# Performance work log

Hardware: AMD Instinct MI355X
Metric: run time of the kernel (lower is better)

Reference implementation:

```python
import jax, jax.numpy as jnp
import numpy as np

B, T, DMODEL = 2, 2048, 1024
H, DK, DV = 16, 64, 64
FF = 4096
EPS = 1e-5


def _layernorm_2d(x):
    # torch LayerNorm(normalized_shape=(T, dmodel)): normalize jointly over last two
    # dims, biased variance, weight=1 / bias=0 (freshly constructed each forward).
    mu = jnp.mean(x, axis=(1, 2), keepdims=True)
    var = jnp.mean((x - mu) ** 2, axis=(1, 2), keepdims=True)
    return (x - mu) / jnp.sqrt(var + EPS)


def setup_inputs() -> dict:
    key = jax.random.key(0)
    ks = jax.random.split(key, 9)
    s = 0.02  # small init for numerical sanity (original uses uniform(-1,1))
    return {
        "x": jax.random.normal(ks[0], (B, T, DMODEL), jnp.float32),
        "Wq": jax.random.normal(ks[1], (H, DMODEL, DK), jnp.float32) * s,
        "Wk": jax.random.normal(ks[2], (H, DMODEL, DK), jnp.float32) * s,
        "Wv": jax.random.normal(ks[3], (H, DMODEL, DV), jnp.float32) * s,
        "Wo": jax.random.normal(ks[4], (DMODEL, DMODEL), jnp.float32) * s,
        "W1": jax.random.normal(ks[5], (DMODEL, FF), jnp.float32) * s,
        "b1": jnp.zeros((FF,), jnp.float32),
        "W2": jax.random.normal(ks[6], (FF, DMODEL), jnp.float32) * s,
        "b2": jnp.zeros((DMODEL,), jnp.float32),
    }


def reference(x, Wq, Wk, Wv, Wo, W1, b1, W2, b2):
    b, t, d = x.shape
    h, _, dk = Wq.shape
    dv = Wv.shape[-1]
    # per-head projections: (B,H,T,dk/dv)
    Qp = jnp.einsum("btd,hdk->bhtk", x, Wq)
    Kp = jnp.einsum("btd,hdk->bhtk", x, Wk)
    Vp = jnp.einsum("btd,hdv->bhtv", x, Wv)
    scores = jnp.einsum("bhqk,bhsk->bhqs", Qp, Kp) / np.sqrt(dk).astype(np.float32)
    # NOTE: original does torch.softmax(heads, 2) -> softmax over the QUERY axis
    attn = jax.nn.softmax(scores, axis=2)
    heads = jnp.einsum("bhqs,bhsv->bqhv", attn, Vp).reshape(b, t, h * dv)
    att_out = heads @ Wo
    o1 = _layernorm_2d(x + att_out)
    ff = jnp.maximum(o1 @ W1 + b1, 0.0) @ W2 + b2
    return _layernorm_2d(o1 + ff)
```

## Files before the change

kernel.cpp:

```cpp
#include <hip/hip_runtime.h>
#include <hip/hip_bf16.h>
#include <cstddef>
#include <cstdint>

typedef __hip_bfloat16 hbf;
typedef __attribute__((ext_vector_type(8))) __bf16 bf16x8;
typedef __attribute__((ext_vector_type(4))) float f32x4;

#define B_ 2
#define T_ 2048
#define D_ 1024
#define H_ 16
#define FF_ 4096
#define EPS_ 1e-5f
#define SCALE_ 0.18033688011112f

__device__ __forceinline__ float bf2f(hbf v) { return __bfloat162float(v); }
__device__ __forceinline__ float fexp2(float x) {
  return __builtin_amdgcn_exp2f(x);
}
__device__ __forceinline__ float flog2(float x) {
  return __builtin_amdgcn_logf(x);
}
__device__ __forceinline__ float ldin(const void* p, size_t i, int isbf) {
  return isbf ? __bfloat162float(((const hbf*)p)[i]) : ((const float*)p)[i];
}
__device__ __forceinline__ void ston(void* p, size_t i, float v, int isbf) {
  if (isbf) ((hbf*)p)[i] = __float2bfloat16(v);
  else ((float*)p)[i] = v;
}
__device__ __forceinline__ f32x4 mfma16(bf16x8 a, bf16x8 b, f32x4 c) {
  return __builtin_amdgcn_mfma_f32_16x16x32_bf16(a, b, c, 0, 0, 0);
}
__device__ __forceinline__ bf16x8 ldfrag(const hbf* p) {
  return *(const bf16x8*)p;
}
__device__ __forceinline__ void glds16(const hbf* g, hbf* l) {
  __builtin_amdgcn_global_load_lds(
      (const __attribute__((address_space(1))) void*)g,
      (__attribute__((address_space(3))) void*)l, 16, 0, 0);
}

__global__ __launch_bounds__(256) void detect_dtype(const unsigned* x,
                                                    int* flag) {
  __shared__ int cnt[256];
  int c = 0;
  for (int i = threadIdx.x; i < 4096; i += 256) {
    unsigned low = x[i] & 0xFFFFu;
    unsigned e = (low >> 7) & 0xFFu;
    if (e >= 100u && e <= 142u) c++;
  }
  cnt[threadIdx.x] = c;
  __syncthreads();
  for (int off = 128; off > 0; off >>= 1) {
    if ((int)threadIdx.x < off) cnt[threadIdx.x] += cnt[threadIdx.x + off];
    __syncthreads();
  }
  if (threadIdx.x == 0) *flag = (cnt[0] > 2458) ? 1 : 0;
}

__device__ __forceinline__ void tr_tile(const void* __restrict__ src,
                                        hbf* __restrict__ dst, int R, int C,
                                        size_t zoff, int cx, int ry, int f,
                                        float (*tile)[33]) {
  const int tx = threadIdx.x & 31, ty = threadIdx.x >> 5;
  const int c0 = cx * 32, r0 = ry * 32;
#pragma unroll
  for (int p = 0; p < 4; p++) {
    int rr = p * 8 + ty;
    tile[rr][tx] = ldin(src, zoff + (size_t)(r0 + rr) * C + c0 + tx, f);
  }
  __syncthreads();
#pragma unroll
  for (int p = 0; p < 4; p++) {
    int cc = p * 8 + ty;
    dst[zoff + (size_t)(c0 + cc) * R + r0 + tx] = __float2bfloat16(tile[tx][cc]);
  }
}

__global__ __launch_bounds__(256) void preconv(
    const void* __restrict__ x, const void* __restrict__ Wq,
    const void* __restrict__ Wk, const void* __restrict__ Wv,
    const void* __restrict__ Wo, const void* __restrict__ W1,
    const void* __restrict__ W2, const void* __restrict__ b1,
    const void* __restrict__ b2, hbf* __restrict__ xb,
    hbf* __restrict__ wqkvt, hbf* __restrict__ wot, hbf* __restrict__ w1t,
    hbf* __restrict__ w2t, hbf* __restrict__ b1b, hbf* __restrict__ b2b,
    const int* __restrict__ flag) {
  __shared__ float tile[32][33];
  const int f = *flag;
  const int bid = blockIdx.x;
  if (bid < 3072) {
    int which = bid >> 10;
    int r = bid & 1023;
    int z = r >> 6, rem = r & 63;
    int ry = rem >> 1, cx = rem & 1;
    const void* src = (which == 0) ? Wq : (which == 1) ? Wk : Wv;
    hbf* dst = wqkvt + (size_t)which * (D_ * D_);
    tr_tile(src, dst, 1024, 64, (size_t)z * 65536, cx, ry, f, tile);
  } else if (bid < 4096) {
    int t = bid - 3072;
    tr_tile(Wo, wot, 1024, 1024, 0, t & 31, t >> 5, f, tile);
  } else if (bid < 8192) {
    int t = bid - 4096;
    tr_tile(W1, w1t, 1024, 4096, 0, t & 127, t >> 7, f, tile);
  } else if (bid < 12288) {
    int t = bid - 8192;
    tr_tile(W2, w2t, 4096, 1024, 0, t & 31, t >> 5, f, tile);
  } else if (bid < 13312) {
    size_t base = (size_t)(bid - 12288) * 4096;
    if (f) {
      const uint4* src = (const uint4*)((const hbf*)x + base);
      uint4* dst = (uint4*)(xb + base);
      for (int i = threadIdx.x; i < 512; i += 256) dst[i] = src[i];
    } else {
      const float4* src = (const float4*)((const float*)x + base);
      for (int i = threadIdx.x; i < 512; i += 256) {
        float4 a = src[i * 2], b = src[i * 2 + 1];
        union {
          hbf h[8];
          uint4 u;
        } o;
        o.h[0] = __float2bfloat16(a.x);
        o.h[1] = __float2bfloat16(a.y);
        o.h[2] = __float2bfloat16(a.z);
        o.h[3] = __float2bfloat16(a.w);
        o.h[4] = __float2bfloat16(b.x);
        o.h[5] = __float2bfloat16(b.y);
        o.h[6] = __float2bfloat16(b.z);
        o.h[7] = __float2bfloat16(b.w);
        *(uint4*)(xb + base + (size_t)i * 8) = o.u;
      }
    }
  } else if (bid == 13312) {
    for (int i = threadIdx.x; i < FF_; i += 256)
      b1b[i] = __float2bfloat16(ldin(b1, i, f));
  } else {
    for (int i = threadIdx.x; i < D_; i += 256)
      b2b[i] = __float2bfloat16(ldin(b2, i, f));
  }
}

template <int MODE, int BM, int BN>
__global__ __launch_bounds__(256) void gemm_bt(
    const hbf* __restrict__ A, const hbf* __restrict__ Bt, hbf* __restrict__ C,
    float* __restrict__ Cf0, float* __restrict__ Cf1,
    const hbf* __restrict__ e1, float* __restrict__ red, int M, int N, int K,
    int LDK) {
  constexpr int WM = BM / 2, WN = BN / 2;
  constexpr int IF = WM / 16, JF = WN / 16;
  __shared__ alignas(16) hbf As[BM * 64];
  __shared__ alignas(16) hbf Bs[BN * 64];
  const int tid = threadIdx.x;
  const int wave = tid >> 6, lane = tid & 63;
  const int quad = lane >> 4, l16 = lane & 15;
  const int m0 = blockIdx.y * BM, n0 = blockIdx.x * BN;
  const int mw = (wave >> 1) * WM, nw = (wave & 1) * WN;
  const int srow = tid >> 3;
  const int scol = (tid & 7) * 8;
  const int kbase = (MODE == 4) ? blockIdx.z * K : 0;
  const f32x4 zero = {0.f, 0.f, 0.f, 0.f};
  f32x4 acc[IF][JF];
#pragma unroll
  for (int i = 0; i < IF; i++)
#pragma unroll
    for (int j = 0; j < JF; j++) acc[i][j] = zero;

  const hbf* ga = &A[(size_t)(m0 + srow) * LDK + kbase + scol];
  const hbf* gb = &Bt[(size_t)(n0 + srow) * LDK + kbase + scol];
  hbf* lA = &As[wave * 512];
  hbf* lB = &Bs[wave * 512];

  for (int k0 = 0; k0 < K; k0 += 64) {
#pragma unroll
    for (int c = 0; c < BM / 32; c++)
      glds16(ga + (size_t)(c * 32) * LDK + k0, lA + c * 2048);
#pragma unroll
    for (int c = 0; c < BN / 32; c++)
      glds16(gb + (size_t)(c * 32) * LDK + k0, lB + c * 2048);
    __syncthreads();
    bf16x8 af[2][IF], bfr[2][JF];
#pragma unroll
    for (int h = 0; h < 2; h++) {
#pragma unroll
      for (int i = 0; i < IF; i++)
        af[h][i] = ldfrag(&As[(mw + i * 16 + l16) * 64 + h * 32 + quad * 8]);
#pragma unroll
      for (int j = 0; j < JF; j++)
        bfr[h][j] = ldfrag(&Bs[(nw + j * 16 + l16) * 64 + h * 32 + quad * 8]);
    }
#pragma unroll
    for (int h = 0; h < 2; h++)
#pragma unroll
      for (int i = 0; i < IF; i++)
#pragma unroll
        for (int j = 0; j < JF; j++)
          acc[i][j] = mfma16(af[h][i], bfr[h][j], acc[i][j]);
    __syncthreads();
  }
  float ssum = 0.f, ssq = 0.f;
#pragma unroll
  for (int i = 0; i < IF; i++)
#pragma unroll
    for (int j = 0; j < JF; j++)
#pragma unroll
      for (int r = 0; r < 4; r++) {
        int m = m0 + mw + i * 16 + quad * 4 + r;
        int n = n0 + nw + j * 16 + l16;
        float v = acc[i][j][r];
        if (MODE == 0) {
          int which = n >> 10, n1 = n & 1023;
          int h = n1 >> 6, cc = n1 & 63;
          int b = m >> 11, t = m & (T_ - 1);
          if (which == 0) v *= SCALE_;
          C[(size_t)which * ((size_t)B_ * H_ * T_ * 64) +
            (((size_t)(b * H_ + h)) * T_ + t) * 64 + cc] = __float2bfloat16(v);
        } else if (MODE == 1) {
          hbf hv = __float2bfloat16(v + bf2f(e1[(size_t)m * N + n]));
          C[(size_t)m * N + n] = hv;
          float fv = bf2f(hv);
          ssum += fv;
          ssq += fv * fv;
        } else if (MODE == 2) {
          C[(size_t)m * N + n] = __float2bfloat16(fmaxf(v + bf2f(e1[n]), 0.f));
        } else if (MODE == 4) {
          float* Cf = blockIdx.z ? Cf1 : Cf0;
          Cf[(size_t)m * N + n] = v;
        }
      }
  if (MODE == 1) {
    float* sc = (float*)As;
    sc[tid] = ssum;
    sc[256 + tid] = ssq;
    __syncthreads();
    for (int off = 128; off > 0; off >>= 1) {
      if (tid < off) {
        sc[tid] += sc[tid + off];
        sc[256 + tid] += sc[256 + tid + off];
      }
      __syncthreads();
    }
    if (tid == 0) {
      int b = m0 >> 11;
      atomicAdd(&red[b * 2 + 0], sc[0]);
      atomicAdd(&red[b * 2 + 1], sc[256]);
    }
  }
}

__global__ __launch_bounds__(256) void attn_stats(const hbf* __restrict__ Q,
                                                  const hbf* __restrict__ K,
                                                  const hbf* __restrict__ V,
                                                  hbf* __restrict__ Vt) {
  __shared__ alignas(16) hbf Ks[64 * 72];
  __shared__ alignas(16) hbf Qs[64 * 72];
  __shared__ float sAdj[64];
  const int bh = blockIdx.y;
  const int s0 = blockIdx.x * 64;
  const int tid = threadIdx.x;
  const int wave = tid >> 6, lane = tid & 63;
  const int quad = lane >> 4, l16 = lane & 15;
  const int sw = wave * 16;
  const hbf* Kb = K + (size_t)bh * T_ * 64;
  const hbf* Qb = Q + (size_t)bh * T_ * 64;
  const hbf* Vb = V + (size_t)bh * T_ * 64;
  hbf* Vtb = Vt + (size_t)bh * 64 * T_;
  const int r_ = tid >> 3, c_ = (tid & 7) * 8;
#pragma unroll
  for (int c = 0; c < 2; c++) {
    int row = c * 32 + r_;
    *(float4*)(&Ks[row * 72 + c_]) =
        *(const float4*)(&Kb[(size_t)(s0 + row) * 64 + c_]);
  }
  __syncthreads();
  bf16x8 kf0 = ldfrag(&Ks[(sw + l16) * 72 + quad * 8]);
  bf16x8 kf1 = ldfrag(&Ks[(sw + l16) * 72 + 32 + quad * 8]);
  float m_thr[4], l_thr[4];
#pragma unroll
  for (int r = 0; r < 4; r++) {
    m_thr[r] = -1e30f;
    l_thr[r] = 0.f;
  }
  const f32x4 zero = {0.f, 0.f, 0.f, 0.f};
  for (int qt = 0; qt < T_ / 64; qt++) {
    if (qt) __syncthreads();
#pragma unroll
    for (int c = 0; c < 2; c++) {
      int row = c * 32 + r_;
      *(float4*)(&Qs[row * 72 + c_]) =
          *(const float4*)(&Qb[(size_t)(qt * 64 + row) * 64 + c_]);
    }
    __syncthreads();
    f32x4 acc[4];
#pragma unroll
    for (int j = 0; j < 4; j++) {
      bf16x8 qf0 = ldfrag(&Qs[(j * 16 + l16) * 72 + quad * 8]);
      bf16x8 qf1 = ldfrag(&Qs[(j * 16 + l16) * 72 + 32 + quad * 8]);
      f32x4 a = zero;
      a = mfma16(kf0, qf0, a);
      a = mfma16(kf1, qf1, a);
      acc[j] = a;
    }
#pragma unroll
    for (int r = 0; r < 4; r++) {
      float mt = fmaxf(fmaxf(acc[0][r], acc[1][r]),
                       fmaxf(acc[2][r], acc[3][r]));
      float nm = fmaxf(m_thr[r], mt);
      float s = l_thr[r] * fexp2(m_thr[r] - nm);
#pragma unroll
      for (int j = 0; j < 4; j++) s += fexp2(acc[j][r] - nm);
      l_thr[r] = s;
      m_thr[r] = nm;
    }
  }
#pragma unroll
  for (int d = 1; d < 16; d <<= 1) {
#pragma unroll
    for (int r = 0; r < 4; r++) {
      float om = __shfl_xor(m_thr[r], d);
      float ol = __shfl_xor(l_thr[r], d);
      float nm = fmaxf(m_thr[r], om);
      l_thr[r] = l_thr[r] * fexp2(m_thr[r] - nm) + ol * fexp2(om - nm);
      m_thr[r] = nm;
    }
  }
  if (l16 == 0) {
#pragma unroll
    for (int r = 0; r < 4; r++)
      sAdj[sw + quad * 4 + r] = m_thr[r] + flog2(l_thr[r]);
  }
  __syncthreads();
#pragma unroll
  for (int c = 0; c < 2; c++) {
    int e = (c * 256 + tid) * 8;
    int r = e >> 6, col = e & 63;
    union alignas(16) {
      hbf h[8];
      float4 f4;
    } u;
    u.f4 = *(const float4*)(&Vb[(size_t)(s0 + r) * 64 + col]);
    float sc = fexp2(-sAdj[r]);
#pragma unroll
    for (int k2 = 0; k2 < 8; k2++)
      u.h[k2] = __float2bfloat16(bf2f(u.h[k2]) * sc);
    *(float4*)(&Ks[r * 72 + col]) = u.f4;
  }
  __syncthreads();
#pragma unroll
  for (int c = 0; c < 2; c++) {
    int e = (c * 256 + tid) * 8;
    int v = e >> 6, tt = e & 63;
    union alignas(16) {
      hbf h[8];
      float4 f4;
    } u;
#pragma unroll
    for (int k2 = 0; k2 < 8; k2++) u.h[k2] = Ks[(tt + k2) * 72 + v];
    *(float4*)(&Vtb[(size_t)v * T_ + s0 + tt]) = u.f4;
  }
}

__global__ __launch_bounds__(256) void attn_apply(const hbf* __restrict__ Q,
                                                  const hbf* __restrict__ K,
                                                  const hbf* __restrict__ Vt,
                                                  hbf* __restrict__ heads) {
  __shared__ alignas(16) hbf Ksb[2 * 64 * 64];
  __shared__ alignas(16) hbf Vsb[3 * 64 * 64];
  __shared__ alignas(16) hbf Ps[4 * 2 * 32 * 72];
  const int bh = blockIdx.y;
  const int b = bh >> 4, h = bh & 15;
  const int q0 = blockIdx.x * 128;
  const int tid = threadIdx.x;
  const int wave = tid >> 6, lane = tid & 63;
  const int quad = lane >> 4, l16 = lane & 15;
  const int qw = wave * 32;
  const hbf* Qb = Q + (size_t)bh * T_ * 64;
  const hbf* Kb = K + (size_t)bh * T_ * 64;
  const hbf* Vtb = Vt + (size_t)bh * 64 * T_;
  hbf* Pw = &Ps[wave * (2 * 32 * 72)];
  const int srow = tid >> 3, sc8 = tid & 7;
  const int swz = sc8 ^ (srow & 7);
  const hbf* gk = Kb + (size_t)srow * 64 + swz * 8;
  const hbf* gv = Vtb + (size_t)srow * T_ + swz * 8;
  hbf* lK = &Ksb[wave * 512];
  hbf* lV = &Vsb[wave * 512];
  const int sx = (l16 & 7) * 8;
  bf16x8 qf[2][2];
#pragma unroll
  for (int i = 0; i < 2; i++)
#pragma unroll
    for (int hh = 0; hh < 2; hh++)
      qf[i][hh] = ldfrag(&Qb[(size_t)(q0 + qw + i * 16 + l16) * 64 + hh * 32 +
                             quad * 8]);
  const f32x4 zero = {0.f, 0.f, 0.f, 0.f};
  f32x4 accO[2][4];
#pragma unroll
  for (int i = 0; i < 2; i++)
#pragma unroll
    for (int j = 0; j < 4; j++) accO[i][j] = zero;

  glds16(gk, lK);
  glds16(gk + 2048, lK + 2048);
  glds16(gv, lV);
  glds16(gv + (size_t)32 * T_, lV + 2048);
  glds16(gk + 4096, lK + 4096);
  glds16(gk + 4096 + 2048, lK + 4096 + 2048);
  glds16(gv + 64, lV + 4096);
  glds16(gv + (size_t)32 * T_ + 64, lV + 4096 + 2048);
  __syncthreads();

  {
    const hbf* Kc = &Ksb[0];
    bf16x8 kf[4][2];
#pragma unroll
    for (int j = 0; j < 4; j++)
#pragma unroll
      for (int hh = 0; hh < 2; hh++)
        kf[j][hh] =
            ldfrag(&Kc[(j * 16 + l16) * 64 + ((hh * 32 + quad * 8) ^ sx)]);
    __builtin_amdgcn_s_setprio(1);
    f32x4 accS[2][4];
#pragma unroll
    for (int i = 0; i < 2; i++)
#pragma unroll
      for (int j = 0; j < 4; j++) {
        f32x4 a = mfma16(kf[j][0], qf[i][0], zero);
        accS[i][j] = mfma16(kf[j][1], qf[i][1], a);
      }
    __builtin_amdgcn_s_setprio(0);
#pragma unroll
    for (int i = 0; i < 2; i++)
#pragma unroll
      for (int j = 0; j < 4; j++) {
        union {
          hbf h4[4];
          uint2 u;
        } pk;
#pragma unroll
        for (int r = 0; r < 4; r++)
          pk.h4[r] = __float2bfloat16(fexp2(accS[i][j][r]));
        *(uint2*)&Pw[(i * 16 + l16) * 72 + j * 16 + quad * 4] = pk.u;
      }
  }
  __syncthreads();

  for (int st = 1; st < T_ / 64; st++) {
    const int kcur = st & 1;
    const int pcur = st & 1, pprev = pcur ^ 1;
    const int vprev = (st - 1) % 3;
    if (st < T_ / 64 - 1) {
      const int knxt = (st + 1) & 1, vnxt = (st + 1) % 3;
      size_t ko = (size_t)(st + 1) * 4096;
      glds16(gk + ko, lK + knxt * 4096);
      glds16(gk + ko + 2048, lK + knxt * 4096 + 2048);
      glds16(gv + (st + 1) * 64, lV + vnxt * 4096);
      glds16(gv + (size_t)32 * T_ + (st + 1) * 64, lV + vnxt * 4096 + 2048);
    }
    const hbf* Kc = &Ksb[kcur * 4096];
    const hbf* Vp = &Vsb[vprev * 4096];
    bf16x8 kf[4][2];
#pragma unroll
    for (int j = 0; j < 4; j++)
#pragma unroll
      for (int hh = 0; hh < 2; hh++)
        kf[j][hh] =
            ldfrag(&Kc[(j * 16 + l16) * 64 + ((hh * 32 + quad * 8) ^ sx)]);
    bf16x8 pf[2][2];
#pragma unroll
    for (int i = 0; i < 2; i++)
#pragma unroll
      for (int hh = 0; hh < 2; hh++)
        pf[i][hh] = ldfrag(
            &Pw[pprev * (32 * 72) + (i * 16 + l16) * 72 + hh * 32 + quad * 8]);
    __builtin_amdgcn_s_setprio(1);
#pragma unroll
    for (int j2 = 0; j2 < 4; j2++) {
      bf16x8 vf0 = ldfrag(&Vp[(j2 * 16 + l16) * 64 + ((quad * 8) ^ sx)]);
      bf16x8 vf1 = ldfrag(&Vp[(j2 * 16 + l16) * 64 + ((32 + quad * 8) ^ sx)]);
#pragma unroll
      for (int i = 0; i < 2; i++) {
        accO[i][j2] = mfma16(pf[i][0], vf0, accO[i][j2]);
        accO[i][j2] = mfma16(pf[i][1], vf1, accO[i][j2]);
      }
    }
    f32x4 accS[2][4];
#pragma unroll
    for (int i = 0; i < 2; i++)
#pragma unroll
      for (int j = 0; j < 4; j++) {
        f32x4 a = mfma16(kf[j][0], qf[i][0], zero);
        accS[i][j] = mfma16(kf[j][1], qf[i][1], a);
      }
    __builtin_amdgcn_s_setprio(0);
#pragma unroll
    for (int i = 0; i < 2; i++)
#pragma unroll
      for (int j = 0; j < 4; j++) {
        union {
          hbf h4[4];
          uint2 u;
        } pk;
#pragma unroll
        for (int r = 0; r < 4; r++)
          pk.h4[r] = __float2bfloat16(fexp2(accS[i][j][r]));
        *(uint2*)&Pw[pcur * (32 * 72) + (i * 16 + l16) * 72 + j * 16 +
                     quad * 4] = pk.u;
      }
    __syncthreads();
  }
  {
    const int pl = (T_ / 64 - 1) & 1;
    const hbf* Vp = &Vsb[((T_ / 64 - 1) % 3) * 4096];
    bf16x8 pf[2][2];
#pragma unroll
    for (int i = 0; i < 2; i++)
#pragma unroll
      for (int hh = 0; hh < 2; hh++)
        pf[i][hh] = ldfrag(
            &Pw[pl * (32 * 72) + (i * 16 + l16) * 72 + hh * 32 + quad * 8]);
    __builtin_amdgcn_s_setprio(1);
#pragma unroll
    for (int j2 = 0; j2 < 4; j2++) {
      bf16x8 vf0 = ldfrag(&Vp[(j2 * 16 + l16) * 64 + ((quad * 8) ^ sx)]);
      bf16x8 vf1 = ldfrag(&Vp[(j2 * 16 + l16) * 64 + ((32 + quad * 8) ^ sx)]);
#pragma unroll
      for (int i = 0; i < 2; i++) {
        accO[i][j2] = mfma16(pf[i][0], vf0, accO[i][j2]);
        accO[i][j2] = mfma16(pf[i][1], vf1, accO[i][j2]);
      }
    }
    __builtin_amdgcn_s_setprio(0);
  }
#pragma unroll
  for (int i = 0; i < 2; i++)
#pragma unroll
    for (int j2 = 0; j2 < 4; j2++)
#pragma unroll
      for (int r = 0; r < 4; r++) {
        int q = q0 + qw + i * 16 + quad * 4 + r;
        int v = j2 * 16 + l16;
        heads[((size_t)(b * T_ + q)) * D_ + h * 64 + v] =
            __float2bfloat16(accO[i][j2][r]);
      }
}

__global__ __launch_bounds__(256) void ln_norm(const hbf* __restrict__ src,
                                               const float* __restrict__ red,
                                               void* dst,
                                               const int* __restrict__ flag,
                                               int force_bf) {
  const int isbf = force_bf ? 1 : *flag;
  const float invN = 1.f / (float)(T_ * D_);
  for (size_t i = (size_t)blockIdx.x * 256 + threadIdx.x;
       i < (size_t)B_ * T_ * D_; i += (size_t)gridDim.x * 256) {
    int b = (int)(i >> 21);
    float mu = red[b * 2 + 0] * invN;
    float var = red[b * 2 + 1] * invN - mu * mu;
    ston(dst, i, (bf2f(src[i]) - mu) * rsqrtf(var + EPS_), isbf);
  }
}

__global__ __launch_bounds__(256) void ln2_stats(const float* __restrict__ P0,
                                                 const float* __restrict__ P1,
                                                 const hbf* __restrict__ o1,
                                                 const hbf* __restrict__ b2b,
                                                 float* __restrict__ red) {
  __shared__ float s1[256], s2[256];
  const int b = blockIdx.y;
  const size_t base = (size_t)b * (T_ * D_);
  float sum = 0.f, sq = 0.f;
  for (size_t i = (size_t)blockIdx.x * 256 + threadIdx.x; i < (size_t)T_ * D_;
       i += (size_t)gridDim.x * 256) {
    size_t e = base + i;
    float v = P0[e] + P1[e] + bf2f(b2b[i & (D_ - 1)]) + bf2f(o1[e]);
    sum += v;
    sq += v * v;
  }
  s1[threadIdx.x] = sum;
  s2[threadIdx.x] = sq;
  __syncthreads();
  for (int off = 128; off > 0; off >>= 1) {
    if ((int)threadIdx.x < off) {
      s1[threadIdx.x] += s1[threadIdx.x + off];
      s2[threadIdx.x] += s2[threadIdx.x + off];
    }
    __syncthreads();
  }
  if (threadIdx.x == 0) {
    atomicAdd(&red[b * 2 + 0], s1[0]);
    atomicAdd(&red[b * 2 + 1], s2[0]);
  }
}

__global__ __launch_bounds__(256) void ln2_norm(
    const float* __restrict__ P0, const float* __restrict__ P1,
    const hbf* __restrict__ o1, const hbf* __restrict__ b2b,
    const float* __restrict__ red, void* dst, const int* __restrict__ flag) {
  const int isbf = *flag;
  const float invN = 1.f / (float)(T_ * D_);
  for (size_t i = (size_t)blockIdx.x * 256 + threadIdx.x;
       i < (size_t)B_ * T_ * D_; i += (size_t)gridDim.x * 256) {
    int b = (int)(i >> 21);
    float mu = red[b * 2 + 0] * invN;
    float var = red[b * 2 + 1] * invN - mu * mu;
    float v = P0[i] + P1[i] + bf2f(b2b[i & (D_ - 1)]) + bf2f(o1[i]);
    ston(dst, i, (v - mu) * rsqrtf(var + EPS_), isbf);
  }
}

extern "C" void kernel_launch(void* const* d_in, const int* in_sizes, int n_in,
                              void* d_out, int out_size, void* d_ws,
                              size_t ws_size, hipStream_t stream) {
  const void* x = d_in[0];
  const void* Wq = d_in[1];
  const void* Wk = d_in[2];
  const void* Wv = d_in[3];
  const void* Wo = d_in[4];
  const void* W1 = d_in[5];
  const void* W2 = d_in[7];
  const void* b1 = d_in[6];
  const void* b2 = d_in[8];

  const size_t MB = 1024 * 1024;
  if (ws_size < 89 * MB) return;

  char* w = (char*)d_ws;
  hbf* xb = (hbf*)(w + 0 * MB);
  hbf* wqkvt = (hbf*)(w + 8 * MB);
  hbf* wot = (hbf*)(w + 14 * MB);
  hbf* w1t = (hbf*)(w + 16 * MB);
  hbf* w2t = (hbf*)(w + 24 * MB);
  hbf* Qb = (hbf*)(w + 32 * MB);
  hbf* Kb = (hbf*)(w + 40 * MB);
  hbf* Vb = (hbf*)(w + 48 * MB);
  hbf* Vtb = (hbf*)(w + 56 * MB);
  hbf* heads = (hbf*)(w + 64 * MB);
  hbf* r1 = (hbf*)(w + 72 * MB);
  hbf* o1 = (hbf*)(w + 80 * MB);
  hbf* ff1 = (hbf*)(w + 32 * MB);
  float* P0 = (float*)(w + 0 * MB);
  float* P1 = (float*)(w + 64 * MB);
  hbf* b1b = (hbf*)(w + 88 * MB);
  hbf* b2b = b1b + FF_;
  float* red = (float*)(b2b + D_);
  int* flag = (int*)(red + 8);

  hipMemsetAsync(red, 0, 8 * sizeof(float) + sizeof(int), stream);
  detect_dtype<<<1, 256, 0, stream>>>((const unsigned*)x, flag);

  const int M = B_ * T_;
  preconv<<<13314, 256, 0, stream>>>(x, Wq, Wk, Wv, Wo, W1, W2, b1, b2, xb,
                                     wqkvt, wot, w1t, w2t, b1b, b2b, flag);
  gemm_bt<0, 128, 128><<<dim3(24, 32), 256, 0, stream>>>(
      xb, wqkvt, Qb, nullptr, nullptr, nullptr, nullptr, M, 3 * D_, D_, D_);
  attn_stats<<<dim3(32, 32), 256, 0, stream>>>(Qb, Kb, Vb, Vtb);
  attn_apply<<<dim3(16, 32), 256, 0, stream>>>(Qb, Kb, Vtb, heads);
  gemm_bt<1, 128, 64><<<dim3(16, 32), 256, 0, stream>>>(
      heads, wot, r1, nullptr, nullptr, xb, red, M, D_, D_, D_);
  ln_norm<<<4096, 256, 0, stream>>>(r1, red, o1, flag, 1);
  gemm_bt<2, 128, 128><<<dim3(32, 32), 256, 0, stream>>>(
      o1, w1t, ff1, nullptr, nullptr, b1b, nullptr, M, FF_, D_, D_);
  gemm_bt<4, 128, 128><<<dim3(8, 32, 2), 256, 0, stream>>>(
      ff1, w2t, nullptr, P0, P1, nullptr, nullptr, M, D_, FF_ / 2, FF_);
  ln2_stats<<<dim3(256, B_), 256, 0, stream>>>(P0, P1, o1, b2b, red + 4);
  ln2_norm<<<2048, 256, 0, stream>>>(P0, P1, o1, b2b, red + 4, d_out, flag);
}
```

Before: 452.5 us.

## Swizzle GEMM block order, transpose MFMA output for vector stores, vectorize LN2

Adds an XCD-aware block-index swizzle to three of the GEMMs so that neighbouring tiles land on the same chiplet, aiming for better L2 reuse. Swaps the MFMA operand order so each lane holds four consecutive columns, which lets every epilogue write packed 8-byte or 16-byte vectors instead of scalar stores. Also vectorizes the final layernorm stats and normalize kernels with float4 and packed bf16 loads and stores. The swizzle assumes the block count divides evenly by 8, and the new output mapping must match the transposed fragment layout.

```diff
diff --git a/kernel.cpp b/kernel.cpp
--- a/kernel.cpp
+++ b/kernel.cpp
@@ -141,7 +141,7 @@
   }
 }
 
-template <int MODE, int BM, int BN>
+template <int MODE, int BM, int BN, int SWZ>
 __global__ __launch_bounds__(256) void gemm_bt(
     const hbf* __restrict__ A, const hbf* __restrict__ Bt, hbf* __restrict__ C,
     float* __restrict__ Cf0, float* __restrict__ Cf1,
@@ -154,7 +154,17 @@
   const int tid = threadIdx.x;
   const int wave = tid >> 6, lane = tid & 63;
   const int quad = lane >> 4, l16 = lane & 15;
-  const int m0 = blockIdx.y * BM, n0 = blockIdx.x * BN;
+  int bx = blockIdx.x, by = blockIdx.y;
+  if (SWZ) {
+    const int gx = gridDim.x;
+    const int nwg = gx * gridDim.y;
+    const int flat = by * gx + bx;
+    const int cpx = nwg >> 3;
+    const int f2 = (flat & 7) * cpx + (flat >> 3);
+    bx = f2 % gx;
+    by = f2 / gx;
+  }
+  const int m0 = by * BM, n0 = bx * BN;
   const int mw = (wave >> 1) * WM, nw = (wave & 1) * WN;
   const int srow = tid >> 3;
   const int scol = (tid & 7) * 8;
@@ -195,39 +205,60 @@
       for (int i = 0; i < IF; i++)
 #pragma unroll
         for (int j = 0; j < JF; j++)
-          acc[i][j] = mfma16(af[h][i], bfr[h][j], acc[i][j]);
+          acc[i][j] = mfma16(bfr[h][j], af[h][i], acc[i][j]);
     __syncthreads();
   }
   float ssum = 0.f, ssq = 0.f;
 #pragma unroll
   for (int i = 0; i < IF; i++)
 #pragma unroll
-    for (int j = 0; j < JF; j++)
-#pragma unroll
-      for (int r = 0; r < 4; r++) {
-        int m = m0 + mw + i * 16 + quad * 4 + r;
-        int n = n0 + nw + j * 16 + l16;
-        float v = acc[i][j][r];
-        if (MODE == 0) {
-          int which = n >> 10, n1 = n & 1023;
-          int h = n1 >> 6, cc = n1 & 63;
-          int b = m >> 11, t = m & (T_ - 1);
-          if (which == 0) v *= SCALE_;
-          C[(size_t)which * ((size_t)B_ * H_ * T_ * 64) +
-            (((size_t)(b * H_ + h)) * T_ + t) * 64 + cc] = __float2bfloat16(v);
-        } else if (MODE == 1) {
-          hbf hv = __float2bfloat16(v + bf2f(e1[(size_t)m * N + n]));
-          C[(size_t)m * N + n] = hv;
+    for (int j = 0; j < JF; j++) {
+      const int m = m0 + mw + i * 16 + l16;
+      const int n = n0 + nw + j * 16 + quad * 4;
+      const f32x4 v = acc[i][j];
+      if (MODE == 0) {
+        int which = n >> 10, n1 = n & 1023;
+        int h = n1 >> 6, cc = n1 & 63;
+        int b = m >> 11, t = m & (T_ - 1);
+        float sc = (which == 0) ? SCALE_ : 1.f;
+        union {
+          hbf h4[4];
+          uint2 u;
+        } pk;
+#pragma unroll
+        for (int r = 0; r < 4; r++) pk.h4[r] = __float2bfloat16(v[r] * sc);
+        *(uint2*)&C[(size_t)which * ((size_t)B_ * H_ * T_ * 64) +
+                    (((size_t)(b * H_ + h)) * T_ + t) * 64 + cc] = pk.u;
+      } else if (MODE == 1) {
+        union {
+          hbf h4[4];
+          uint2 u;
+        } e, o;
+        e.u = *(const uint2*)&e1[(size_t)m * N + n];
+#pragma unroll
+        for (int r = 0; r < 4; r++) {
+          hbf hv = __float2bfloat16(v[r] + bf2f(e.h4[r]));
+          o.h4[r] = hv;
           float fv = bf2f(hv);
           ssum += fv;
           ssq += fv * fv;
-        } else if (MODE == 2) {
-          C[(size_t)m * N + n] = __float2bfloat16(fmaxf(v + bf2f(e1[n]), 0.f));
-        } else if (MODE == 4) {
-          float* Cf = blockIdx.z ? Cf1 : Cf0;
-          Cf[(size_t)m * N + n] = v;
         }
-      }
+        *(uint2*)&C[(size_t)m * N + n] = o.u;
+      } else if (MODE == 2) {
+        union {
+          hbf h4[4];
+          uint2 u;
+        } e, o;
+        e.u = *(const uint2*)&e1[n];
+#pragma unroll
+        for (int r = 0; r < 4; r++)
+          o.h4[r] = __float2bfloat16(fmaxf(v[r] + bf2f(e.h4[r]), 0.f));
+        *(uint2*)&C[(size_t)m * N + n] = o.u;
+      } else if (MODE == 4) {
+        float* Cf = blockIdx.z ? Cf1 : Cf0;
+        *(f32x4*)&Cf[(size_t)m * N + n] = v;
+      }
+    }
   if (MODE == 1) {
     float* sc = (float*)As;
     sc[tid] = ssum;
@@ -567,14 +598,27 @@
                                                  float* __restrict__ red) {
   __shared__ float s1[256], s2[256];
   const int b = blockIdx.y;
-  const size_t base = (size_t)b * (T_ * D_);
+  const size_t base = (size_t)b * (T_ * D_ / 4);
+  const float4* P0v = (const float4*)P0;
+  const float4* P1v = (const float4*)P1;
+  const uint2* o1v = (const uint2*)o1;
+  const uint2* b2v = (const uint2*)b2b;
   float sum = 0.f, sq = 0.f;
-  for (size_t i = (size_t)blockIdx.x * 256 + threadIdx.x; i < (size_t)T_ * D_;
-       i += (size_t)gridDim.x * 256) {
-    size_t e = base + i;
-    float v = P0[e] + P1[e] + bf2f(b2b[i & (D_ - 1)]) + bf2f(o1[e]);
-    sum += v;
-    sq += v * v;
+  for (size_t i = (size_t)blockIdx.x * 256 + threadIdx.x;
+       i < (size_t)(T_ * D_ / 4); i += (size_t)gridDim.x * 256) {
+    float4 p0 = P0v[base + i], p1 = P1v[base + i];
+    union {
+      uint2 u;
+      hbf h[4];
+    } o, bb;
+    o.u = o1v[base + i];
+    bb.u = b2v[i & (D_ / 4 - 1)];
+#pragma unroll
+    for (int r = 0; r < 4; r++) {
+      float v = (&p0.x)[r] + (&p1.x)[r] + bf2f(bb.h[r]) + bf2f(o.h[r]);
+      sum += v;
+      sq += v * v;
+    }
   }
   s1[threadIdx.x] = sum;
   s2[threadIdx.x] = sq;
@@ -598,13 +642,40 @@
     const float* __restrict__ red, void* dst, const int* __restrict__ flag) {
   const int isbf = *flag;
   const float invN = 1.f / (float)(T_ * D_);
+  const float4* P0v = (const float4*)P0;
+  const float4* P1v = (const float4*)P1;
+  const uint2* o1v = (const uint2*)o1;
+  const uint2* b2v = (const uint2*)b2b;
   for (size_t i = (size_t)blockIdx.x * 256 + threadIdx.x;
-       i < (size_t)B_ * T_ * D_; i += (size_t)gridDim.x * 256) {
-    int b = (int)(i >> 21);
+       i < (size_t)B_ * T_ * D_ / 4; i += (size_t)gridDim.x * 256) {
+    int b = (int)(i >> 19);
     float mu = red[b * 2 + 0] * invN;
     float var = red[b * 2 + 1] * invN - mu * mu;
-    float v = P0[i] + P1[i] + bf2f(b2b[i & (D_ - 1)]) + bf2f(o1[i]);
-    ston(dst, i, (v - mu) * rsqrtf(var + EPS_), isbf);
+    float rstd = rsqrtf(var + EPS_);
+    float4 p0 = P0v[i], p1 = P1v[i];
+    union {
+      uint2 u;
+      hbf h[4];
+    } o, bb;
+    o.u = o1v[i];
+    bb.u = b2v[i & (D_ / 4 - 1)];
+    float out[4];
+#pragma unroll
+    for (int r = 0; r < 4; r++)
+      out[r] =
+          ((&p0.x)[r] + (&p1.x)[r] + bf2f(bb.h[r]) + bf2f(o.h[r]) - mu) * rstd;
+    if (isbf) {
+      union {
+        hbf h[4];
+        uint2 u;
+      } pk;
+#pragma unroll
+      for (int r = 0; r < 4; r++) pk.h[r] = __float2bfloat16(out[r]);
+      ((uint2*)dst)[i] = pk.u;
+    } else {
+      float4 f{out[0], out[1], out[2], out[3]};
+      ((float4*)dst)[i] = f;
+    }
   }
 }
 
@@ -651,16 +722,16 @@
   const int M = B_ * T_;
   preconv<<<13314, 256, 0, stream>>>(x, Wq, Wk, Wv, Wo, W1, W2, b1, b2, xb,
                                      wqkvt, wot, w1t, w2t, b1b, b2b, flag);
-  gemm_bt<0, 128, 128><<<dim3(24, 32), 256, 0, stream>>>(
+  gemm_bt<0, 128, 128, 1><<<dim3(24, 32), 256, 0, stream>>>(
       xb, wqkvt, Qb, nullptr, nullptr, nullptr, nullptr, M, 3 * D_, D_, D_);
   attn_stats<<<dim3(32, 32), 256, 0, stream>>>(Qb, Kb, Vb, Vtb);
   attn_apply<<<dim3(16, 32), 256, 0, stream>>>(Qb, Kb, Vtb, heads);
-  gemm_bt<1, 128, 64><<<dim3(16, 32), 256, 0, stream>>>(
+  gemm_bt<1, 128, 64, 0><<<dim3(16, 32), 256, 0, stream>>>(
       heads, wot, r1, nullptr, nullptr, xb, red, M, D_, D_, D_);
   ln_norm<<<4096, 256, 0, stream>>>(r1, red, o1, flag, 1);
-  gemm_bt<2, 128, 128><<<dim3(32, 32), 256, 0, stream>>>(
+  gemm_bt<2, 128, 128, 1><<<dim3(32, 32), 256, 0, stream>>>(
       o1, w1t, ff1, nullptr, nullptr, b1b, nullptr, M, FF_, D_, D_);
-  gemm_bt<4, 128, 128><<<dim3(8, 32, 2), 256, 0, stream>>>(
+  gemm_bt<4, 128, 128, 1><<<dim3(8, 32, 2), 256, 0, stream>>>(
       ff1, w2t, nullptr, P0, P1, nullptr, nullptr, M, D_, FF_ / 2, FF_);
   ln2_stats<<<dim3(256, B_), 256, 0, stream>>>(P0, P1, o1, b2b, red + 4);
   ln2_norm<<<2048, 256, 0, stream>>>(P0, P1, o1, b2b, red + 4, d_out, flag);
```

Measured after the change: 462.6 us. 1.02x slower.
